# Performance work log

Hardware: AMD Instinct MI355X
Metric: run time of the kernel (lower is better)

The kernel has to match this reference:

```python
import jax, jax.numpy as jnp
import numpy as np

V, F, N = 5143, 10144, 2_000_000


def _safe_normalize(x):
    # matches GaussianAvatars safe_normalize: x / sqrt(clamp(|x|^2, min=1e-20))
    return x * jax.lax.rsqrt(jnp.clip(jnp.sum(x * x, axis=-1, keepdims=True), 1e-20, None))


def _quat_wxyz_to_rotmat(q):
    # rotation_activation (L2 normalize with eps) then wxyz->xyzw + roma unitquat_to_rotmat
    q = q / (jnp.sqrt(jnp.sum(q * q, axis=-1, keepdims=True)) + 1e-12)
    w, x, y, z = q[..., 0], q[..., 1], q[..., 2], q[..., 3]
    R = jnp.stack([
        jnp.stack([1 - 2 * (y * y + z * z), 2 * (x * y - z * w), 2 * (x * z + y * w)], axis=-1),
        jnp.stack([2 * (x * y + z * w), 1 - 2 * (x * x + z * z), 2 * (y * z - x * w)], axis=-1),
        jnp.stack([2 * (x * z - y * w), 2 * (y * z + x * w), 1 - 2 * (x * x + y * y)], axis=-1),
    ], axis=-2)
    return R  # [N,3,3]


def setup_inputs() -> dict:
    key = jax.random.key(0)
    ks = jax.random.split(key, 9)
    verts = jax.random.normal(ks[0], (V, 3), jnp.float32) * 0.1
    faces = jax.random.randint(ks[1], (F, 3), 0, V, dtype=jnp.int32)
    binding = jax.random.randint(ks[2], (N,), 0, F, dtype=jnp.int32)
    xyz = jax.random.normal(ks[3], (N, 3), jnp.float32) * 0.01
    rotation = jax.random.normal(ks[4], (N, 4), jnp.float32)
    scaling = jax.random.normal(ks[5], (N, 3), jnp.float32) - 4.0
    opacity = jax.random.normal(ks[6], (N, 1), jnp.float32)
    features_dc = jax.random.normal(ks[7], (N, 1, 3), jnp.float32)
    features_rest = jax.random.normal(ks[8], (N, 15, 3), jnp.float32) * 0.1
    return dict(verts=verts, faces=faces, binding=binding, xyz=xyz, rotation=rotation,
                scaling=scaling, opacity=opacity, features_dc=features_dc,
                features_rest=features_rest)


def reference(verts, faces, binding, xyz, rotation, scaling, opacity, features_dc, features_rest):
    # --- per-face geometry (compute_face_orientation + face_center) ---
    v0 = verts[faces[:, 0]]  # [F,3]
    v1 = verts[faces[:, 1]]
    v2 = verts[faces[:, 2]]
    face_center = (v0 + v1 + v2) / 3.0  # triangles.mean(dim=-2)
    e01 = v1 - v0
    e02 = v2 - v0
    a0 = _safe_normalize(e01)
    a1 = _safe_normalize(jnp.cross(a0, e02))
    a2 = -_safe_normalize(jnp.cross(a1, a0))
    face_orien_mat = jnp.stack([a0, a1, a2], axis=-1)  # [F,3,3], columns = axes
    s0 = jnp.sqrt(jnp.sum(e01 * e01, axis=-1, keepdims=True))
    s1 = jnp.abs(jnp.sum(a2 * e02, axis=-1, keepdims=True))
    face_scaling = 0.5 * (s0 + s1)  # [F,1]

    # --- binding-indexed gathers ---
    O_b = face_orien_mat[binding]      # [N,3,3]
    fs_b = face_scaling[binding]       # [N,1]
    fc_b = face_center[binding]        # [N,3]

    # --- gaussian position in world space ---
    xyz_out = jnp.einsum('nij,nj->ni', O_b, xyz) * fs_b + fc_b  # [N,3]

    # --- color (dc sh band 0 + opacity), scaled to 0..255 ---
    op = jax.nn.sigmoid(opacity)  # [N,1]
    color = jnp.clip((jnp.concatenate([0.5 + 0.282 * features_dc[:, 0, :], op], axis=-1)) * 255.0, 0.0, 255.0)

    # --- covariance build ---
    scales = jnp.exp(scaling) * fs_b  # [N,3]
    Q = _quat_wxyz_to_rotmat(rotation)  # [N,3,3]
    rotations = jnp.swapaxes(jnp.einsum('nij,njk->nik', O_b, Q), 1, 2)  # (O@Q)^T, [N,3,3]
    sig = rotations * scales[:, :, None]  # einsum('bij,bi->bij')
    C = jnp.einsum('nij,nik->njk', sig, sig)  # [N,3,3] = sig^T sig
    simga = jnp.stack([C[:, 0, 0], C[:, 0, 1], C[:, 0, 2], C[:, 1, 1], C[:, 1, 2], C[:, 2, 2]], axis=-1)

    return jnp.concatenate([xyz_out, color, simga], axis=-1)  # [N,13]
```

## Files before the change

### kernel.cpp

```cpp
#include <hip/hip_runtime.h>
#include <math.h>

struct F3 { float x, y, z; };

__device__ __forceinline__ F3 f3(float x, float y, float z) { return {x, y, z}; }
__device__ __forceinline__ F3 add(F3 a, F3 b) { return {a.x+b.x, a.y+b.y, a.z+b.z}; }
__device__ __forceinline__ F3 sub(F3 a, F3 b) { return {a.x-b.x, a.y-b.y, a.z-b.z}; }
__device__ __forceinline__ F3 mul(F3 a, float s) { return {a.x*s, a.y*s, a.z*s}; }
__device__ __forceinline__ float dot3(F3 a, F3 b) { return a.x*b.x + a.y*b.y + a.z*b.z; }
__device__ __forceinline__ F3 cross3(F3 a, F3 b) {
    return {a.y*b.z - a.z*b.y, a.z*b.x - a.x*b.z, a.x*b.y - a.y*b.x};
}
__device__ __forceinline__ F3 safe_normalize(F3 a) {
    float d = dot3(a, a);
    float inv = rsqrtf(fmaxf(d, 1e-20f));
    return mul(a, inv);
}

#define BLK 256

__global__ __launch_bounds__(BLK) void gauss_fused_kernel(
    const float* __restrict__ verts,
    const int*   __restrict__ faces,
    const int*   __restrict__ binding,
    const float* __restrict__ xyz,
    const float* __restrict__ rot,
    const float* __restrict__ scal,
    const float* __restrict__ opac,
    const float* __restrict__ fdc,
    float*       __restrict__ out,
    int N)
{
    __shared__ float sout[BLK * 13];

    const int tid = threadIdx.x;
    const int i  = blockIdx.x * BLK + tid;
    const int count = min(BLK, N - blockIdx.x * BLK);

    if (i < N) {
        const int b = binding[i];
        const int f0 = faces[3*b+0], f1 = faces[3*b+1], f2 = faces[3*b+2];
        const F3 v0 = f3(verts[3*f0], verts[3*f0+1], verts[3*f0+2]);
        const F3 v1 = f3(verts[3*f1], verts[3*f1+1], verts[3*f1+2]);
        const F3 v2 = f3(verts[3*f2], verts[3*f2+1], verts[3*f2+2]);

        const F3 fc  = mul(add(add(v0, v1), v2), (1.0f/3.0f));
        const F3 e01 = sub(v1, v0);
        const F3 e02 = sub(v2, v0);
        const F3 a0 = safe_normalize(e01);
        const F3 a1 = safe_normalize(cross3(a0, e02));
        const F3 a2 = mul(safe_normalize(cross3(a1, a0)), -1.0f);
        const float s0 = sqrtf(dot3(e01, e01));
        const float s1 = fabsf(dot3(a2, e02));
        const float fs = 0.5f * (s0 + s1);

        const float px = xyz[3*i+0], py = xyz[3*i+1], pz = xyz[3*i+2];
        const float4 q4 = reinterpret_cast<const float4*>(rot)[i];
        const float sc0 = scal[3*i+0], sc1 = scal[3*i+1], sc2 = scal[3*i+2];
        const float opa = opac[i];
        const float d0 = fdc[3*i+0], d1 = fdc[3*i+1], d2 = fdc[3*i+2];

        F3 xo = add(add(mul(a0, px), mul(a1, py)), mul(a2, pz));
        xo = add(mul(xo, fs), fc);

        const float qn = sqrtf(q4.x*q4.x + q4.y*q4.y + q4.z*q4.z + q4.w*q4.w) + 1e-12f;
        const float qinv = 1.0f / qn;
        const float w = q4.x*qinv, x = q4.y*qinv, y = q4.z*qinv, z = q4.w*qinv;
        const float Q00 = 1.0f - 2.0f*(y*y + z*z);
        const float Q01 = 2.0f*(x*y - z*w);
        const float Q02 = 2.0f*(x*z + y*w);
        const float Q10 = 2.0f*(x*y + z*w);
        const float Q11 = 1.0f - 2.0f*(x*x + z*z);
        const float Q12 = 2.0f*(y*z - x*w);
        const float Q20 = 2.0f*(x*z - y*w);
        const float Q21 = 2.0f*(y*z + x*w);
        const float Q22 = 1.0f - 2.0f*(x*x + y*y);

        const F3 m0 = add(add(mul(a0, Q00), mul(a1, Q10)), mul(a2, Q20));
        const F3 m1 = add(add(mul(a0, Q01), mul(a1, Q11)), mul(a2, Q21));
        const F3 m2 = add(add(mul(a0, Q02), mul(a1, Q12)), mul(a2, Q22));

        const float w0 = expf(sc0) * fs;
        const float w1 = expf(sc1) * fs;
        const float w2 = expf(sc2) * fs;
        const float t0 = w0*w0, t1 = w1*w1, t2 = w2*w2;

        const float C00 = t0*m0.x*m0.x + t1*m1.x*m1.x + t2*m2.x*m2.x;
        const float C01 = t0*m0.x*m0.y + t1*m1.x*m1.y + t2*m2.x*m2.y;
        const float C02 = t0*m0.x*m0.z + t1*m1.x*m1.z + t2*m2.x*m2.z;
        const float C11 = t0*m0.y*m0.y + t1*m1.y*m1.y + t2*m2.y*m2.y;
        const float C12 = t0*m0.y*m0.z + t1*m1.y*m1.z + t2*m2.y*m2.z;
        const float C22 = t0*m0.z*m0.z + t1*m1.z*m1.z + t2*m2.z*m2.z;

        const float sg = 1.0f / (1.0f + expf(-opa));
        const float c0 = fminf(fmaxf((0.5f + 0.282f*d0) * 255.0f, 0.0f), 255.0f);
        const float c1 = fminf(fmaxf((0.5f + 0.282f*d1) * 255.0f, 0.0f), 255.0f);
        const float c2 = fminf(fmaxf((0.5f + 0.282f*d2) * 255.0f, 0.0f), 255.0f);
        const float c3 = fminf(fmaxf(sg * 255.0f, 0.0f), 255.0f);

        float r[13] = {xo.x, xo.y, xo.z, c0, c1, c2, c3, C00, C01, C02, C11, C12, C22};
        #pragma unroll
        for (int j = 0; j < 13; ++j) sout[tid*13 + j] = r[j];
    }

    __syncthreads();

    const int total = count * 13;
    const size_t base = (size_t)blockIdx.x * (BLK * 13);
    const int n4 = total >> 2;
    const float4* s4 = reinterpret_cast<const float4*>(sout);
    float4* o4 = reinterpret_cast<float4*>(out + base);
    for (int j = tid; j < n4; j += BLK) o4[j] = s4[j];
    for (int j = (n4 << 2) + tid; j < total; j += BLK) out[base + j] = sout[j];
}

extern "C" void kernel_launch(void* const* d_in, const int* in_sizes, int n_in,
                              void* d_out, int out_size, void* d_ws, size_t ws_size,
                              hipStream_t stream) {
    const float* verts   = (const float*)d_in[0];
    const int*   faces   = (const int*)  d_in[1];
    const int*   binding = (const int*)  d_in[2];
    const float* xyz     = (const float*)d_in[3];
    const float* rot     = (const float*)d_in[4];
    const float* scal    = (const float*)d_in[5];
    const float* opac    = (const float*)d_in[6];
    const float* fdc     = (const float*)d_in[7];
    float* out = (float*)d_out;
    const int N = in_sizes[2];

    const int blocks = (N + BLK - 1) / BLK;
    gauss_fused_kernel<<<blocks, BLK, 0, stream>>>(
        verts, faces, binding, xyz, rot, scal, opac, fdc, out, N);
}
```

Baseline: 48.97 us.

## Precompute per-face frame table in a separate kernel before the main gather

Adds a face precompute kernel that computes each face's center, scale and orthonormal frame once and stores them as four float4 entries in workspace. The main kernel then gathers the table through the binding index instead of doing a double indirection through faces and verts and recomputing the normalisations for every gaussian. This cuts redundant per-point ALU work and dependent scattered loads, at the cost of an extra launch and a 64-byte gather per point. A fallback to the original fused kernel is kept for when workspace is too small.

New measurement: 45.02 us. 1.09x faster.

```diff
diff --git a/kernel.cpp b/kernel.cpp
--- a/kernel.cpp
+++ b/kernel.cpp
@@ -19,20 +19,130 @@
 
 #define BLK 256
 
-__global__ __launch_bounds__(BLK) void gauss_fused_kernel(
-    const float* __restrict__ verts,
-    const int*   __restrict__ faces,
-    const int*   __restrict__ binding,
-    const float* __restrict__ xyz,
-    const float* __restrict__ rot,
-    const float* __restrict__ scal,
-    const float* __restrict__ opac,
-    const float* __restrict__ fdc,
-    float*       __restrict__ out,
+__global__ __launch_bounds__(BLK) void face_precompute_kernel(
+    const float* __restrict__ verts, const int* __restrict__ faces,
+    float4* __restrict__ tab, int F)
+{
+    const int f = blockIdx.x * BLK + threadIdx.x;
+    if (f >= F) return;
+    const int f0 = faces[3*f+0], f1 = faces[3*f+1], f2 = faces[3*f+2];
+    const F3 v0 = f3(verts[3*f0], verts[3*f0+1], verts[3*f0+2]);
+    const F3 v1 = f3(verts[3*f1], verts[3*f1+1], verts[3*f1+2]);
+    const F3 v2 = f3(verts[3*f2], verts[3*f2+1], verts[3*f2+2]);
+
+    const F3 fc  = mul(add(add(v0, v1), v2), (1.0f/3.0f));
+    const F3 e01 = sub(v1, v0);
+    const F3 e02 = sub(v2, v0);
+    const F3 a0 = safe_normalize(e01);
+    const F3 a1 = safe_normalize(cross3(a0, e02));
+    const F3 a2 = mul(safe_normalize(cross3(a1, a0)), -1.0f);
+    const float s0 = sqrtf(dot3(e01, e01));
+    const float s1 = fabsf(dot3(a2, e02));
+    const float fs = 0.5f * (s0 + s1);
+
+    tab[4*f+0] = make_float4(fc.x, fc.y, fc.z, fs);
+    tab[4*f+1] = make_float4(a0.x, a0.y, a0.z, 0.0f);
+    tab[4*f+2] = make_float4(a1.x, a1.y, a1.z, 0.0f);
+    tab[4*f+3] = make_float4(a2.x, a2.y, a2.z, 0.0f);
+}
+
+__global__ __launch_bounds__(BLK) void gauss_main_kernel(
+    const float4* __restrict__ tab,
+    const int*    __restrict__ binding,
+    const float*  __restrict__ xyz,
+    const float*  __restrict__ rot,
+    const float*  __restrict__ scal,
+    const float*  __restrict__ opac,
+    const float*  __restrict__ fdc,
+    float*        __restrict__ out,
     int N)
 {
     __shared__ float sout[BLK * 13];
 
+    const int tid = threadIdx.x;
+    const int i  = blockIdx.x * BLK + tid;
+    const int count = min(BLK, N - blockIdx.x * BLK);
+
+    if (i < N) {
+        const int b = binding[i];
+        const float4 t0 = tab[4*b+0];
+        const float4 t1 = tab[4*b+1];
+        const float4 t2 = tab[4*b+2];
+        const float4 t3 = tab[4*b+3];
+        const F3 fc = f3(t0.x, t0.y, t0.z);
+        const float fs = t0.w;
+        const F3 a0 = f3(t1.x, t1.y, t1.z);
+        const F3 a1 = f3(t2.x, t2.y, t2.z);
+        const F3 a2 = f3(t3.x, t3.y, t3.z);
+
+        const float px = xyz[3*i+0], py = xyz[3*i+1], pz = xyz[3*i+2];
+        const float4 q4 = reinterpret_cast<const float4*>(rot)[i];
+        const float sc0 = scal[3*i+0], sc1 = scal[3*i+1], sc2 = scal[3*i+2];
+        const float opa = opac[i];
+        const float d0 = fdc[3*i+0], d1 = fdc[3*i+1], d2 = fdc[3*i+2];
+
+        F3 xo = add(add(mul(a0, px), mul(a1, py)), mul(a2, pz));
+        xo = add(mul(xo, fs), fc);
+
+        const float qn = sqrtf(q4.x*q4.x + q4.y*q4.y + q4.z*q4.z + q4.w*q4.w) + 1e-12f;
+        const float qinv = 1.0f / qn;
+        const float w = q4.x*qinv, x = q4.y*qinv, y = q4.z*qinv, z = q4.w*qinv;
+        const float Q00 = 1.0f - 2.0f*(y*y + z*z);
+        const float Q01 = 2.0f*(x*y - z*w);
+        const float Q02 = 2.0f*(x*z + y*w);
+        const float Q10 = 2.0f*(x*y + z*w);
+        const float Q11 = 1.0f - 2.0f*(x*x + z*z);
+        const float Q12 = 2.0f*(y*z - x*w);
+        const float Q20 = 2.0f*(x*z - y*w);
+        const float Q21 = 2.0f*(y*z + x*w);
+        const float Q22 = 1.0f - 2.0f*(x*x + y*y);
+
+        const F3 m0 = add(add(mul(a0, Q00), mul(a1, Q10)), mul(a2, Q20));
+        const F3 m1 = add(add(mul(a0, Q01), mul(a1, Q11)), mul(a2, Q21));
+        const F3 m2 = add(add(mul(a0, Q02), mul(a1, Q12)), mul(a2, Q22));
+
+        const float w0 = expf(sc0) * fs;
+        const float w1 = expf(sc1) * fs;
+        const float w2 = expf(sc2) * fs;
+        const float t0s = w0*w0, t1s = w1*w1, t2s = w2*w2;
+
+        const float C00 = t0s*m0.x*m0.x + t1s*m1.x*m1.x + t2s*m2.x*m2.x;
+        const float C01 = t0s*m0.x*m0.y + t1s*m1.x*m1.y + t2s*m2.x*m2.y;
+        const float C02 = t0s*m0.x*m0.z + t1s*m1.x*m1.z + t2s*m2.x*m2.z;
+        const float C11 = t0s*m0.y*m0.y + t1s*m1.y*m1.y + t2s*m2.y*m2.y;
+        const float C12 = t0s*m0.y*m0.z + t1s*m1.y*m1.z + t2s*m2.y*m2.z;
+        const float C22 = t0s*m0.z*m0.z + t1s*m1.z*m1.z + t2s*m2.z*m2.z;
+
+        const float sg = 1.0f / (1.0f + expf(-opa));
+        const float c0 = fminf(fmaxf((0.5f + 0.282f*d0) * 255.0f, 0.0f), 255.0f);
+        const float c1 = fminf(fmaxf((0.5f + 0.282f*d1) * 255.0f, 0.0f), 255.0f);
+        const float c2 = fminf(fmaxf((0.5f + 0.282f*d2) * 255.0f, 0.0f), 255.0f);
+        const float c3 = fminf(fmaxf(sg * 255.0f, 0.0f), 255.0f);
+
+        float r[13] = {xo.x, xo.y, xo.z, c0, c1, c2, c3, C00, C01, C02, C11, C12, C22};
+        #pragma unroll
+        for (int j = 0; j < 13; ++j) sout[tid*13 + j] = r[j];
+    }
+
+    __syncthreads();
+
+    const int total = count * 13;
+    const size_t base = (size_t)blockIdx.x * (BLK * 13);
+    const int n4 = total >> 2;
+    const float4* s4 = reinterpret_cast<const float4*>(sout);
+    float4* o4 = reinterpret_cast<float4*>(out + base);
+    for (int j = tid; j < n4; j += BLK) o4[j] = s4[j];
+    for (int j = (n4 << 2) + tid; j < total; j += BLK) out[base + j] = sout[j];
+}
+
+__global__ __launch_bounds__(BLK) void gauss_fused_kernel(
+    const float* __restrict__ verts, const int* __restrict__ faces,
+    const int* __restrict__ binding, const float* __restrict__ xyz,
+    const float* __restrict__ rot, const float* __restrict__ scal,
+    const float* __restrict__ opac, const float* __restrict__ fdc,
+    float* __restrict__ out, int N)
+{
+    __shared__ float sout[BLK * 13];
     const int tid = threadIdx.x;
     const int i  = blockIdx.x * BLK + tid;
     const int count = min(BLK, N - blockIdx.x * BLK);
@@ -43,7 +153,6 @@
         const F3 v0 = f3(verts[3*f0], verts[3*f0+1], verts[3*f0+2]);
         const F3 v1 = f3(verts[3*f1], verts[3*f1+1], verts[3*f1+2]);
         const F3 v2 = f3(verts[3*f2], verts[3*f2+1], verts[3*f2+2]);
-
         const F3 fc  = mul(add(add(v0, v1), v2), (1.0f/3.0f));
         const F3 e01 = sub(v1, v0);
         const F3 e02 = sub(v2, v0);
@@ -127,8 +236,19 @@
     const float* fdc     = (const float*)d_in[7];
     float* out = (float*)d_out;
     const int N = in_sizes[2];
-
+    const int F = in_sizes[1] / 3;
+
+    const size_t tab_bytes = (size_t)F * 4 * sizeof(float4);
     const int blocks = (N + BLK - 1) / BLK;
-    gauss_fused_kernel<<<blocks, BLK, 0, stream>>>(
-        verts, faces, binding, xyz, rot, scal, opac, fdc, out, N);
-}
+
+    if (ws_size >= tab_bytes) {
+        float4* tab = (float4*)d_ws;
+        const int fblocks = (F + BLK - 1) / BLK;
+        face_precompute_kernel<<<fblocks, BLK, 0, stream>>>(verts, faces, tab, F);
+        gauss_main_kernel<<<blocks, BLK, 0, stream>>>(
+            tab, binding, xyz, rot, scal, opac, fdc, out, N);
+    } else {
+        gauss_fused_kernel<<<blocks, BLK, 0, stream>>>(
+            verts, faces, binding, xyz, rot, scal, opac, fdc, out, N);
+    }
+}
```
